# Kernel tuning notes

Measured on AMD Instinct MI355X. Metric: run time of the kernel, lower is better.

## Reference

```python
import jax, jax.numpy as jnp
import numpy as np

EPS = 1e-5  # torch BatchNorm1d default eps
NBLK = 4    # number of crops
BLK = 10    # block size (40/4)


def setup_inputs() -> dict:
    key = jax.random.key(0)
    k1, k2, k3 = jax.random.split(key, 3)
    B, N, Fin, Fout = 8192, 40, 256, 256
    inp = jax.random.normal(k1, (B, N, Fin), dtype=jnp.float32)
    adj = jax.random.uniform(k2, (B, N, N), dtype=jnp.float32)
    stdv = 1.0 / np.sqrt(Fout)
    W = jax.random.uniform(k3, (Fin, Fout), dtype=jnp.float32, minval=-stdv, maxval=stdv)
    bn_gamma = jnp.ones((NBLK, N * Fout), dtype=jnp.float32)
    bn_beta = jnp.zeros((NBLK, N * Fout), dtype=jnp.float32)
    return {"input": inp, "adj": adj, "W": W, "bn_gamma": bn_gamma, "bn_beta": bn_beta}


def reference(input, adj, W, bn_gamma, bn_beta):
    B, N, _ = input.shape
    Fout = W.shape[1]
    support = jnp.einsum('bnf,fo->bno', input, W)  # [B, N, Fout]
    out = jnp.zeros((B, N, Fout), dtype=input.dtype)
    for i in range(NBLK):
        s, e = i * BLK, (i + 1) * BLK
        # adj * block_mask then bmm == bmm restricted to the diagonal block
        blk = jnp.einsum('bij,bjo->bio', adj[:, s:e, s:e], support[:, s:e, :])  # [B,10,Fout]
        full = jnp.zeros((B, N, Fout), dtype=input.dtype).at[:, s:e, :].set(blk)
        flat = full.reshape(B, N * Fout)
        # BatchNorm1d in training mode: biased batch stats over the batch dim
        mean = jnp.mean(flat, axis=0)
        var = jnp.var(flat, axis=0)
        normed = (flat - mean) * jax.lax.rsqrt(var + EPS) * bn_gamma[i] + bn_beta[i]
        out = out + normed.reshape(B, N, Fout)
    # out_mask is all ones -> identity
    return out
```

## Files before the change

### kernel.cpp

```cpp
#include <hip/hip_runtime.h>
#include <stdint.h>

#define B_    8192
#define N_    40
#define F_    256
#define NBLK_ 4
#define BLK_  10
#define M_    (B_*N_)
#define NF_   (N_*F_)

using frag_t = __attribute__((ext_vector_type(8))) short;
using f32x4  = __attribute__((ext_vector_type(4))) float;

__device__ __forceinline__ unsigned short f2b(float x){
  unsigned int u = __float_as_uint(x);
  u += 0x7FFF + ((u >> 16) & 1);
  return (unsigned short)(u >> 16);
}
__device__ __forceinline__ float b2f(unsigned short h){
  return __uint_as_float(((unsigned int)h) << 16);
}

__global__ __launch_bounds__(256) void k_prep(const float* __restrict__ W,
                                              unsigned short* __restrict__ Wt,
                                              float* __restrict__ sums){
  int id = blockIdx.x*256 + threadIdx.x;
  int f = id >> 8, k = id & 255;
  Wt[f*256 + k] = f2b(W[k*256 + f]);
  if (id < 2*NF_) sums[id] = 0.f;
}

__global__ __launch_bounds__(256) void k_aprime(const float* __restrict__ input,
                                                const float* __restrict__ adj,
                                                unsigned short* __restrict__ A){
  int bb = blockIdx.x; int b = bb >> 2; int s = (bb & 3) * BLK_;
  int f = threadIdx.x;
  __shared__ float sadj[BLK_*BLK_];
  if (f < BLK_*BLK_){
    int n = f / 10, j = f - n*10;
    sadj[f] = adj[b*1600 + (s + n)*40 + (s + j)];
  }
  __syncthreads();
  float acc[BLK_];
  #pragma unroll
  for (int n = 0; n < BLK_; ++n) acc[n] = 0.f;
  const float* ip = input + (size_t)(b*N_ + s)*F_ + f;
  #pragma unroll
  for (int j = 0; j < BLK_; ++j){
    float x = ip[j*F_];
    #pragma unroll
    for (int n = 0; n < BLK_; ++n) acc[n] += sadj[n*10 + j] * x;
  }
  unsigned short* op = A + (size_t)(b*N_ + s)*F_ + f;
  #pragma unroll
  for (int n = 0; n < BLK_; ++n) op[n*F_] = f2b(acc[n]);
}

__global__ __launch_bounds__(256, 2) void k_gemm(unsigned short* __restrict__ A,
                                                 const unsigned short* __restrict__ Wt){
  __shared__ unsigned short As[128][136];
  const int t    = threadIdx.x;
  const int m0   = blockIdx.x * 128;
  const int lane = t & 63, wave = t >> 6;
  const int wr   = (wave >> 1) * 64;
  const int wc   = (wave & 1) * 128;
  const int lm   = lane & 15;
  const int lq   = lane >> 4;
  const int lk8  = lq * 8;

  f32x4 acc[4][8];
  #pragma unroll
  for (int i = 0; i < 4; ++i)
    #pragma unroll
    for (int j = 0; j < 8; ++j)
      acc[i][j] = (f32x4){0.f, 0.f, 0.f, 0.f};

  const unsigned short* Ag = A + (size_t)m0 * 256;
  const int sr = t >> 4, sc = t & 15;

  for (int kh = 0; kh < 2; ++kh){
    __syncthreads();
    #pragma unroll
    for (int it = 0; it < 8; ++it){
      int r = it*16 + sr;
      uint4 v = *(const uint4*)(Ag + r*256 + kh*128 + sc*8);
      *(uint4*)(&As[r][sc*8]) = v;
    }
    __syncthreads();
    #pragma unroll
    for (int kc = 0; kc < 4; ++kc){
      frag_t av[4], bv[8];
      #pragma unroll
      for (int rt = 0; rt < 4; ++rt)
        av[rt] = *(const frag_t*)(&As[wr + rt*16 + lm][kc*32 + lk8]);
      const unsigned short* wp = Wt + (size_t)(wc + lm)*256 + kh*128 + kc*32 + lk8;
      #pragma unroll
      for (int ct = 0; ct < 8; ++ct)
        bv[ct] = *(const frag_t*)(wp + ct*16*256);
      #pragma unroll
      for (int rt = 0; rt < 4; ++rt)
        #pragma unroll
        for (int ct = 0; ct < 8; ++ct)
          acc[rt][ct] = __builtin_amdgcn_mfma_f32_16x16x32_bf16(av[rt], bv[ct], acc[rt][ct], 0, 0, 0);
    }
  }
  #pragma unroll
  for (int rt = 0; rt < 4; ++rt)
    #pragma unroll
    for (int ct = 0; ct < 8; ++ct){
      int gr = wr + rt*16 + lq*4;
      int gc = wc + ct*16 + lm;
      #pragma unroll
      for (int r = 0; r < 4; ++r)
        A[(size_t)(m0 + gr + r)*256 + gc] = f2b(acc[rt][ct][r]);
    }
}

__global__ __launch_bounds__(256) void k_stats(const unsigned short* __restrict__ A,
                                               float* __restrict__ sums){
  int n = blockIdx.x % 40, sl = blockIdx.x / 40;
  int f = threadIdx.x;
  float s = 0.f, ss = 0.f;
  int b0 = sl * 256;
  for (int b = b0; b < b0 + 256; ++b){
    float v = b2f(A[(size_t)(b*N_ + n)*256 + f]);
    s += v; ss += v*v;
  }
  atomicAdd(&sums[n*256 + f], s);
  atomicAdd(&sums[NF_ + n*256 + f], ss);
}

__global__ __launch_bounds__(256) void k_finalize(const float* __restrict__ sums,
                                                  const float* __restrict__ gamma,
                                                  const float* __restrict__ beta,
                                                  float* __restrict__ st){
  int nf = blockIdx.x*256 + threadIdx.x;
  int n = nf >> 8;
  int blki = n / 10;
  float mean = sums[nf] * (1.f/8192.f);
  float var  = sums[NF_ + nf] * (1.f/8192.f) - mean*mean;
  float sc = gamma[blki*NF_ + nf] * rsqrtf(var + 1e-5f);
  float tt = -mean * sc;
  #pragma unroll
  for (int i = 0; i < 4; ++i) tt += beta[i*NF_ + nf];
  st[nf] = sc;
  st[NF_ + nf] = tt;
}

__global__ __launch_bounds__(256) void k_norm(const unsigned short* __restrict__ A,
                                              const float* __restrict__ st,
                                              float* __restrict__ out){
  size_t idx = ((size_t)blockIdx.x*256 + threadIdx.x) * 8;
  uint4 raw = *(const uint4*)(A + idx);
  int nf = (int)(idx % NF_);
  const float4 s0 = *(const float4*)(st + nf);
  const float4 s1 = *(const float4*)(st + nf + 4);
  const float4 t0 = *(const float4*)(st + NF_ + nf);
  const float4 t1 = *(const float4*)(st + NF_ + nf + 4);
  float4 o0, o1;
  o0.x = b2f((unsigned short)(raw.x & 0xFFFF)) * s0.x + t0.x;
  o0.y = b2f((unsigned short)(raw.x >> 16))    * s0.y + t0.y;
  o0.z = b2f((unsigned short)(raw.y & 0xFFFF)) * s0.z + t0.z;
  o0.w = b2f((unsigned short)(raw.y >> 16))    * s0.w + t0.w;
  o1.x = b2f((unsigned short)(raw.z & 0xFFFF)) * s1.x + t1.x;
  o1.y = b2f((unsigned short)(raw.z >> 16))    * s1.y + t1.y;
  o1.z = b2f((unsigned short)(raw.w & 0xFFFF)) * s1.z + t1.z;
  o1.w = b2f((unsigned short)(raw.w >> 16))    * s1.w + t1.w;
  *(float4*)(out + idx)     = o0;
  *(float4*)(out + idx + 4) = o1;
}

extern "C" void kernel_launch(void* const* d_in, const int* in_sizes, int n_in,
                              void* d_out, int out_size, void* d_ws, size_t ws_size,
                              hipStream_t stream){
  const float* input = (const float*)d_in[0];
  const float* adj   = (const float*)d_in[1];
  const float* W     = (const float*)d_in[2];
  const float* gamma = (const float*)d_in[3];
  const float* beta  = (const float*)d_in[4];
  float* out = (float*)d_out;

  char* ws = (char*)d_ws;
  unsigned short* A  = (unsigned short*)ws;
  unsigned short* Wt = (unsigned short*)(ws + (size_t)M_*256*2);
  float* sums = (float*)(ws + (size_t)M_*256*2 + 256*256*2);
  float* st   = sums + 2*NF_;

  k_prep    <<<256,        256, 0, stream>>>(W, Wt, sums);
  k_aprime  <<<B_*NBLK_,   256, 0, stream>>>(input, adj, A);
  k_gemm    <<<M_/128,     256, 0, stream>>>(A, Wt);
  k_stats   <<<40*32,      256, 0, stream>>>(A, sums);
  k_finalize<<<NF_/256,    256, 0, stream>>>(sums, gamma, beta, st);
  k_norm    <<<(int)(((size_t)M_*256)/2048), 256, 0, stream>>>(A, st, out);
}
```

Baseline: 827.6 us.

## Fuse adjacency aggregation, projection GEMM and batch statistics into one kernel

```diff
diff --git a/kernel.cpp b/kernel.cpp
--- a/kernel.cpp
+++ b/kernel.cpp
@@ -8,6 +8,8 @@
 #define BLK_  10
 #define M_    (B_*N_)
 #define NF_   (N_*F_)
+#define BG_   8
+#define ROWS_ (BG_*BLK_)
 
 using frag_t = __attribute__((ext_vector_type(8))) short;
 using f32x4  = __attribute__((ext_vector_type(4))) float;
@@ -30,104 +32,123 @@
   if (id < 2*NF_) sums[id] = 0.f;
 }
 
-__global__ __launch_bounds__(256) void k_aprime(const float* __restrict__ input,
-                                                const float* __restrict__ adj,
-                                                unsigned short* __restrict__ A){
-  int bb = blockIdx.x; int b = bb >> 2; int s = (bb & 3) * BLK_;
-  int f = threadIdx.x;
-  __shared__ float sadj[BLK_*BLK_];
-  if (f < BLK_*BLK_){
-    int n = f / 10, j = f - n*10;
-    sadj[f] = adj[b*1600 + (s + n)*40 + (s + j)];
-  }
-  __syncthreads();
-  float acc[BLK_];
-  #pragma unroll
-  for (int n = 0; n < BLK_; ++n) acc[n] = 0.f;
-  const float* ip = input + (size_t)(b*N_ + s)*F_ + f;
-  #pragma unroll
-  for (int j = 0; j < BLK_; ++j){
-    float x = ip[j*F_];
-    #pragma unroll
-    for (int n = 0; n < BLK_; ++n) acc[n] += sadj[n*10 + j] * x;
-  }
-  unsigned short* op = A + (size_t)(b*N_ + s)*F_ + f;
-  #pragma unroll
-  for (int n = 0; n < BLK_; ++n) op[n*F_] = f2b(acc[n]);
-}
-
-__global__ __launch_bounds__(256, 2) void k_gemm(unsigned short* __restrict__ A,
-                                                 const unsigned short* __restrict__ Wt){
-  __shared__ unsigned short As[128][136];
-  const int t    = threadIdx.x;
-  const int m0   = blockIdx.x * 128;
+__global__ __launch_bounds__(256, 2) void k_fused(const float* __restrict__ input,
+                                                  const float* __restrict__ adj,
+                                                  const unsigned short* __restrict__ Wt,
+                                                  unsigned short* __restrict__ A,
+                                                  float* __restrict__ sums){
+  __shared__ __align__(16) float sadjp[BG_][BLK_][12];
+  __shared__ __align__(16) unsigned short As[ROWS_][264];
+
+  const int t  = threadIdx.x;
+  const int wg = blockIdx.x;
+  const int b0 = (wg >> 2) * BG_;
+  const int s  = (wg & 3) * BLK_;
+
+  for (int i = t; i < BG_*100; i += 256){
+    int bl = i / 100, r = i - bl*100;
+    int n = r / 10, j = r - n*10;
+    sadjp[bl][n][j] = adj[(size_t)(b0+bl)*(N_*N_) + (s+n)*N_ + (s+j)];
+  }
+  __syncthreads();
+
+  {
+    const int bl = t >> 5, u = t & 31;
+    const float* ip0 = input + ((size_t)(b0+bl)*N_ + s)*F_ + u*4;
+    #pragma unroll
+    for (int kh = 0; kh < 2; ++kh){
+      float4 x[BLK_];
+      #pragma unroll
+      for (int j = 0; j < BLK_; ++j)
+        x[j] = *(const float4*)(ip0 + kh*128 + j*F_);
+      #pragma unroll
+      for (int n = 0; n < BLK_; ++n){
+        const float4 cA = *(const float4*)(&sadjp[bl][n][0]);
+        const float4 cB = *(const float4*)(&sadjp[bl][n][4]);
+        const float2 cC = *(const float2*)(&sadjp[bl][n][8]);
+        const float c[10] = {cA.x,cA.y,cA.z,cA.w,cB.x,cB.y,cB.z,cB.w,cC.x,cC.y};
+        float ax=0.f, ay=0.f, az=0.f, aw=0.f;
+        #pragma unroll
+        for (int j = 0; j < BLK_; ++j){
+          ax += c[j]*x[j].x; ay += c[j]*x[j].y;
+          az += c[j]*x[j].z; aw += c[j]*x[j].w;
+        }
+        uint2 p;
+        p.x = (unsigned)f2b(ax) | ((unsigned)f2b(ay) << 16);
+        p.y = (unsigned)f2b(az) | ((unsigned)f2b(aw) << 16);
+        *(uint2*)(&As[bl*BLK_ + n][kh*128 + u*4]) = p;
+      }
+    }
+  }
+  __syncthreads();
+
   const int lane = t & 63, wave = t >> 6;
-  const int wr   = (wave >> 1) * 64;
-  const int wc   = (wave & 1) * 128;
+  const int wc   = wave * 64;
   const int lm   = lane & 15;
   const int lq   = lane >> 4;
   const int lk8  = lq * 8;
 
-  f32x4 acc[4][8];
-  #pragma unroll
-  for (int i = 0; i < 4; ++i)
-    #pragma unroll
-    for (int j = 0; j < 8; ++j)
+  f32x4 acc[5][4];
+  #pragma unroll
+  for (int i = 0; i < 5; ++i)
+    #pragma unroll
+    for (int j = 0; j < 4; ++j)
       acc[i][j] = (f32x4){0.f, 0.f, 0.f, 0.f};
 
-  const unsigned short* Ag = A + (size_t)m0 * 256;
-  const int sr = t >> 4, sc = t & 15;
-
+  #pragma unroll
   for (int kh = 0; kh < 2; ++kh){
-    __syncthreads();
-    #pragma unroll
-    for (int it = 0; it < 8; ++it){
-      int r = it*16 + sr;
-      uint4 v = *(const uint4*)(Ag + r*256 + kh*128 + sc*8);
-      *(uint4*)(&As[r][sc*8]) = v;
-    }
-    __syncthreads();
     #pragma unroll
     for (int kc = 0; kc < 4; ++kc){
-      frag_t av[4], bv[8];
-      #pragma unroll
-      for (int rt = 0; rt < 4; ++rt)
-        av[rt] = *(const frag_t*)(&As[wr + rt*16 + lm][kc*32 + lk8]);
+      frag_t av[5], bv[4];
+      #pragma unroll
+      for (int rt = 0; rt < 5; ++rt)
+        av[rt] = *(const frag_t*)(&As[rt*16 + lm][kh*128 + kc*32 + lk8]);
       const unsigned short* wp = Wt + (size_t)(wc + lm)*256 + kh*128 + kc*32 + lk8;
       #pragma unroll
-      for (int ct = 0; ct < 8; ++ct)
+      for (int ct = 0; ct < 4; ++ct)
         bv[ct] = *(const frag_t*)(wp + ct*16*256);
       #pragma unroll
-      for (int rt = 0; rt < 4; ++rt)
+      for (int rt = 0; rt < 5; ++rt)
         #pragma unroll
-        for (int ct = 0; ct < 8; ++ct)
+        for (int ct = 0; ct < 4; ++ct)
           acc[rt][ct] = __builtin_amdgcn_mfma_f32_16x16x32_bf16(av[rt], bv[ct], acc[rt][ct], 0, 0, 0);
     }
   }
-  #pragma unroll
-  for (int rt = 0; rt < 4; ++rt)
-    #pragma unroll
-    for (int ct = 0; ct < 8; ++ct){
-      int gr = wr + rt*16 + lq*4;
-      int gc = wc + ct*16 + lm;
+  __syncthreads();
+
+  #pragma unroll
+  for (int rt = 0; rt < 5; ++rt)
+    #pragma unroll
+    for (int ct = 0; ct < 4; ++ct)
       #pragma unroll
       for (int r = 0; r < 4; ++r)
-        A[(size_t)(m0 + gr + r)*256 + gc] = f2b(acc[rt][ct][r]);
+        As[rt*16 + lq*4 + r][wc + ct*16 + lm] = f2b(acc[rt][ct][r]);
+  __syncthreads();
+
+  float sm[BLK_], sq[BLK_];
+  #pragma unroll
+  for (int n = 0; n < BLK_; ++n){ sm[n] = 0.f; sq[n] = 0.f; }
+  #pragma unroll
+  for (int bl = 0; bl < BG_; ++bl)
+    #pragma unroll
+    for (int n = 0; n < BLK_; ++n){
+      float v = b2f(As[bl*BLK_ + n][t]);
+      sm[n] += v; sq[n] += v*v;
     }
-}
-
-__global__ __launch_bounds__(256) void k_stats(const unsigned short* __restrict__ A,
-                                               float* __restrict__ sums){
-  int n = blockIdx.x % 40, sl = blockIdx.x / 40;
-  int f = threadIdx.x;
-  float s = 0.f, ss = 0.f;
-  int b0 = sl * 256;
-  for (int b = b0; b < b0 + 256; ++b){
-    float v = b2f(A[(size_t)(b*N_ + n)*256 + f]);
-    s += v; ss += v*v;
-  }
-  atomicAdd(&sums[n*256 + f], s);
-  atomicAdd(&sums[NF_ + n*256 + f], ss);
+  #pragma unroll
+  for (int n = 0; n < BLK_; ++n){
+    atomicAdd(&sums[(s+n)*F_ + t],        sm[n]);
+    atomicAdd(&sums[NF_ + (s+n)*F_ + t],  sq[n]);
+  }
+
+  #pragma unroll
+  for (int i = 0; i < 10; ++i){
+    int c   = i*256 + t;
+    int row = c >> 5, cc = (c & 31)*8;
+    int q   = row / BLK_, rm = row - q*BLK_;
+    uint4 v = *(const uint4*)(&As[row][cc]);
+    *(uint4*)(A + ((size_t)(b0 + q)*N_ + s + rm)*F_ + cc) = v;
+  }
 }
 
 __global__ __launch_bounds__(256) void k_finalize(const float* __restrict__ sums,
@@ -186,10 +207,8 @@
   float* sums = (float*)(ws + (size_t)M_*256*2 + 256*256*2);
   float* st   = sums + 2*NF_;
 
-  k_prep    <<<256,        256, 0, stream>>>(W, Wt, sums);
-  k_aprime  <<<B_*NBLK_,   256, 0, stream>>>(input, adj, A);
-  k_gemm    <<<M_/128,     256, 0, stream>>>(A, Wt);
-  k_stats   <<<40*32,      256, 0, stream>>>(A, sums);
-  k_finalize<<<NF_/256,    256, 0, stream>>>(sums, gamma, beta, st);
+  k_prep    <<<256,             256, 0, stream>>>(W, Wt, sums);
+  k_fused   <<<(B_/BG_)*NBLK_,  256, 0, stream>>>(input, adj, Wt, A, sums);
+  k_finalize<<<NF_/256,         256, 0, stream>>>(sums, gamma, beta, st);
   k_norm    <<<(int)(((size_t)M_*256)/2048), 256, 0, stream>>>(A, st, out);
 }
```

Measured after the change: 843.5 us. Within noise of the previous version (+1.9%).
